# Kernel optimization log

Hardware: AMD Instinct MI355X
Metric: run time of the kernel (lower is better)

The kernel has to match this reference:

```python
import jax, jax.numpy as jnp
import numpy as np

B, S, D, H = 2, 2048, 1024, 16
HD = D // H  # head_dim = 64


def setup_inputs() -> dict:
    key = jax.random.key(0)
    ks = jax.random.split(key, 11)
    init = 1.0 / np.sqrt(D)
    inp = {
        "query": jax.random.normal(ks[0], (B, S, D), jnp.float32),
        "key": jax.random.normal(ks[1], (B, S, D), jnp.float32),
        "value": jax.random.normal(ks[2], (B, S, D), jnp.float32),
        "Wq": jax.random.uniform(ks[3], (D, D), jnp.float32, -init, init),
        "bq": jax.random.uniform(ks[4], (D,), jnp.float32, -init, init),
        "Wk": jax.random.uniform(ks[5], (D, D), jnp.float32, -init, init),
        "bk": jax.random.uniform(ks[6], (D,), jnp.float32, -init, init),
        "Wv": jax.random.uniform(ks[7], (D, D), jnp.float32, -init, init),
        "bv": jax.random.uniform(ks[8], (D,), jnp.float32, -init, init),
        "Wo": jax.random.uniform(ks[9], (D, D), jnp.float32, -init, init),
        "bo": jax.random.uniform(ks[10], (D,), jnp.float32, -init, init),
    }
    return inp


def reference(query, key, value, Wq, bq, Wk, bk, Wv, bv, Wo, bo):
    # Linear projections (torch Linear: x @ W.T + b)
    q = query @ Wq.T + bq  # [B,S,D]
    k = key @ Wk.T + bk
    v = value @ Wv.T + bv
    # split heads -> [B,H,S,HD]
    q = q.reshape(B, S, H, HD).transpose(0, 2, 1, 3)
    k = k.reshape(B, S, H, HD).transpose(0, 2, 1, 3)
    v = v.reshape(B, S, H, HD).transpose(0, 2, 1, 3)
    # NOTE: original code divides by scale = head_dim**-0.5, i.e. multiplies
    # scores by sqrt(head_dim). Reproduced faithfully.
    scale = HD ** (-0.5)
    scores = jnp.einsum("bhqd,bhkd->bhqk", q, k) / scale  # [B,H,S,S]
    attn = jax.nn.softmax(scores, axis=-1)
    x = jnp.einsum("bhqk,bhkd->bhqd", attn, v)  # [B,H,S,HD]
    x = x.transpose(0, 2, 1, 3).reshape(B, S, D)
    return x @ Wo.T + bo
```

## Files before the change

### kernel.cpp

```cpp
#include <hip/hip_runtime.h>
#include <stdint.h>
#include <stddef.h>

#define SCALE_LOG2E 11.541560327111707f
#define E8 4194304
#define M1 1048576
#define NROW 65536

typedef __attribute__((ext_vector_type(8))) _Float16 f16x8;
typedef __attribute__((ext_vector_type(4))) _Float16 f16x4;
typedef __attribute__((ext_vector_type(4))) float f32x4;

#if __has_builtin(__builtin_amdgcn_exp2f)
#define EXP2F(x) __builtin_amdgcn_exp2f(x)
#else
#define EXP2F(x) exp2f(x)
#endif

__device__ __forceinline__ f32x4 mfma_f16(f16x8 a, f16x8 b, f32x4 c) {
  return __builtin_amdgcn_mfma_f32_16x16x32_f16(a, b, c, 0, 0, 0);
}

__device__ __forceinline__ void async16(const void* g, void* lds) {
  __builtin_amdgcn_global_load_lds(
      (const __attribute__((address_space(1))) unsigned int*)g,
      (__attribute__((address_space(3))) unsigned int*)lds, 16, 0, 0);
}

__global__ void prep_all(const float* __restrict__ q, const float* __restrict__ k,
                         const float* __restrict__ v,
                         const float* __restrict__ wq, const float* __restrict__ wk,
                         const float* __restrict__ wv, const float* __restrict__ wo,
                         _Float16* __restrict__ Xf, _Float16* __restrict__ Wf) {
  const int gid = blockIdx.x;
  const float* src;
  _Float16* dst;
  int i;
  if (gid < 12288) {
    const int z = gid >> 12;
    src = (z == 0) ? q : (z == 1) ? k : v;
    dst = Xf + (size_t)z * E8;
    i = (gid & 4095) * 256 + threadIdx.x;
  } else {
    const int g2 = gid - 12288;
    const int z = g2 >> 10;
    src = (z == 0) ? wq : (z == 1) ? wk : (z == 2) ? wv : wo;
    dst = Wf + (size_t)z * M1;
    i = (g2 & 1023) * 256 + threadIdx.x;
  }
  float4 x = ((const float4*)src)[i];
  f16x4 h = {(_Float16)x.x, (_Float16)x.y, (_Float16)x.z, (_Float16)x.w};
  ((f16x4*)dst)[i] = h;
}

__global__ __launch_bounds__(256, 3) void gemm_qkv(
    const _Float16* __restrict__ Xf,
    const _Float16* __restrict__ Wf,
    const float* __restrict__ bq, const float* __restrict__ bk,
    const float* __restrict__ bv,
    _Float16* __restrict__ Of)
{
  __shared__ _Float16 SMEM[16384];
  _Float16* LA = SMEM;
  _Float16* LB = SMEM + 8192;
  const int z = blockIdx.z;
  const int tid = threadIdx.x;
  const int lane = tid & 63;
  const int wv = tid >> 6;
  const int wm = wv >> 1, wn = wv & 1;
  const int rl = lane & 15, qd = lane >> 4;
  const int m0 = blockIdx.y * 128, n0 = blockIdx.x * 128;

  const _Float16* A0 = Xf + (size_t)z * E8;
  const _Float16* W0 = Wf + (size_t)z * M1;
  const float* bias = (z == 0) ? bq : (z == 1) ? bk : bv;

  f32x4 acc[4][4];
#pragma unroll
  for (int i = 0; i < 4; i++)
#pragma unroll
    for (int j = 0; j < 4; j++) acc[i][j] = f32x4{0.f, 0.f, 0.f, 0.f};

  const int srow = wv * 32 + (lane >> 2);
  const int scol = (lane & 3) * 8;

  auto stage = [&](int k0, int buf) {
    const _Float16* ga = A0 + (size_t)(m0 + srow) * 1024 + k0 + scol;
    async16(ga, &LA[buf * 4096 + wv * 1024]);
    async16(ga + 16 * 1024, &LA[buf * 4096 + wv * 1024 + 512]);
    const _Float16* gb = W0 + (size_t)(n0 + srow) * 1024 + k0 + scol;
    async16(gb, &LB[buf * 4096 + wv * 1024]);
    async16(gb + 16 * 1024, &LB[buf * 4096 + wv * 1024 + 512]);
  };

  stage(0, 0);
  for (int t = 0; t < 32; t++) {
    const int buf = t & 1;
    __syncthreads();
    if (t + 1 < 32) stage((t + 1) * 32, buf ^ 1);
    f16x8 af[4], bfr[4];
#pragma unroll
    for (int i = 0; i < 4; i++) af[i] = *(const f16x8*)&LA[buf * 4096 + (wm * 64 + i * 16 + rl) * 32 + qd * 8];
#pragma unroll
    for (int j = 0; j < 4; j++) bfr[j] = *(const f16x8*)&LB[buf * 4096 + (wn * 64 + j * 16 + rl) * 32 + qd * 8];
#pragma unroll
    for (int i = 0; i < 4; i++)
#pragma unroll
      for (int j = 0; j < 4; j++) acc[i][j] = mfma_f16(af[i], bfr[j], acc[i][j]);
  }

  if (z == 2) {
#pragma unroll
    for (int j = 0; j < 4; j++) {
      const int nn = n0 + wn * 64 + j * 16 + rl;
      const float bj = bias[nn];
      const int hh = nn >> 6, e = nn & 63;
#pragma unroll
      for (int i = 0; i < 4; i++) {
        const int mm = m0 + wm * 64 + i * 16 + qd * 4;
        const int b = mm >> 11, s = mm & 2047;
        f16x4 pk = {(_Float16)(acc[i][j][0] + bj), (_Float16)(acc[i][j][1] + bj),
                    (_Float16)(acc[i][j][2] + bj), (_Float16)(acc[i][j][3] + bj)};
        *(f16x4*)(Of + 2 * (size_t)E8 + (((size_t)((b * 16 + hh) * 64 + e)) << 11) + s) = pk;
      }
    }
  } else {
    const float scl = (z == 0) ? SCALE_LOG2E : 1.0f;
    _Float16* base = Of + (size_t)z * E8;
    __syncthreads();
#pragma unroll
    for (int j = 0; j < 4; j++) {
      const int nl = wn * 64 + j * 16 + rl;
      const float bj = bias[n0 + nl];
#pragma unroll
      for (int i = 0; i < 4; i++) {
        const int ml = wm * 64 + i * 16 + qd * 4;
        const int np = nl ^ (qd << 4);
#pragma unroll
        for (int r = 0; r < 4; r++)
          SMEM[(ml + r) * 128 + np] = (_Float16)((acc[i][j][r] + bj) * scl);
      }
    }
    __syncthreads();
#pragma unroll
    for (int it2 = 0; it2 < 8; it2++) {
      const int m = (it2 * 256 + tid) >> 4;
      const int col8 = (tid & 15) * 8;
      const int np = col8 ^ (((m >> 2) & 3) << 4);
      f16x8 vrow = *(const f16x8*)&SMEM[m * 128 + np];
      const int sg = m0 + m;
      const int b = sg >> 11, s = sg & 2047;
      const int nn = n0 + col8;
      const int hh = nn >> 6, e = nn & 63;
      *(f16x8*)(base + (((size_t)((b * 16 + hh) * 2048 + s)) << 6) + e) = vrow;
    }
  }
}

__global__ __launch_bounds__(256, 3) void attn_kernel(
    const _Float16* __restrict__ Qb,
    const _Float16* __restrict__ Kb,
    const _Float16* __restrict__ Vt,
    float* __restrict__ Op,
    float2* __restrict__ ML)
{
  __shared__ _Float16 Ks[2][4096];
  __shared__ _Float16 Vs[2][4096];
  __shared__ _Float16 Ps[4][32][76];
  const int tid = threadIdx.x;
  const int lane = tid & 63;
  const int wv = tid >> 6;
  const int rl = lane & 15, qd = lane >> 4;
  const int bh = blockIdx.z;
  const int half = blockIdx.y;
  const int kvb = half * 1024;
  const int q0 = blockIdx.x * 128 + wv * 32;

  f16x8 qf[2][2];
#pragma unroll
  for (int mt = 0; mt < 2; mt++)
#pragma unroll
    for (int kk = 0; kk < 2; kk++)
      qf[mt][kk] = *(const f16x8*)(Qb + ((size_t)bh * 2048 + q0 + mt * 16 + rl) * 64 +
                                   kk * 32 + qd * 8);

  float m_[2] = {-1e30f, -1e30f}, l_[2] = {0.f, 0.f};
  f32x4 o[2][4];
#pragma unroll
  for (int mt = 0; mt < 2; mt++)
#pragma unroll
    for (int jt = 0; jt < 4; jt++) o[mt][jt] = f32x4{0.f, 0.f, 0.f, 0.f};

  auto stage = [&](int kv, int buf) {
#pragma unroll
    for (int it = 0; it < 2; it++) {
      const int cI = it * 256 + tid;
      const int row = cI >> 3;
      const int c = (cI & 7) ^ (row & 7);
      const int dst = (it * 256 + wv * 64) * 8;
      async16(Kb + ((size_t)bh * 2048 + kv + row) * 64 + c * 8, &Ks[buf][dst]);
      async16(Vt + ((size_t)bh * 64 + row) * 2048 + kv + c * 8, &Vs[buf][dst]);
    }
  };

  stage(kvb, 0);

  for (int t = 0; t < 16; t++) {
    const int buf = t & 1;
    __syncthreads();
    if (t + 1 < 16) stage(kvb + (t + 1) * 64, buf ^ 1);

    f32x4 sc[2][4];
#pragma unroll
    for (int mt = 0; mt < 2; mt++)
#pragma unroll
      for (int nt = 0; nt < 4; nt++) sc[mt][nt] = f32x4{0.f, 0.f, 0.f, 0.f};
#pragma unroll
    for (int nt = 0; nt < 4; nt++) {
      const int ro = (nt * 16 + rl) * 64;
#pragma unroll
      for (int kk = 0; kk < 2; kk++) {
        const int cc = (((kk * 4 + qd) ^ (rl & 7)) << 3);
        f16x8 kh = *(const f16x8*)&Ks[buf][ro + cc];
#pragma unroll
        for (int mt = 0; mt < 2; mt++)
          sc[mt][nt] = mfma_f16(kh, qf[mt][kk], sc[mt][nt]);
      }
    }

#pragma unroll
    for (int mt = 0; mt < 2; mt++) {
      float mloc = sc[mt][0][0];
#pragma unroll
      for (int nt = 0; nt < 4; nt++)
#pragma unroll
        for (int r = 0; r < 4; r++) mloc = fmaxf(mloc, sc[mt][nt][r]);
      float mx = fmaxf(mloc, __shfl_xor(mloc, 16));
      mx = fmaxf(mx, __shfl_xor(mx, 32));
      float sm = 0.f;
#pragma unroll
      for (int nt = 0; nt < 4; nt++)
#pragma unroll
        for (int r = 0; r < 4; r++) {
          float p = EXP2F(sc[mt][nt][r] - mloc);
          sc[mt][nt][r] = p;
          sm += p;
        }
      const float mold = m_[mt];
      const float mnew = fmaxf(mold, mx);
      m_[mt] = mnew;
      const float cf = EXP2F(mloc - mnew);
      if (__any(mnew > mold)) {
        const float al = EXP2F(mold - mnew);
        l_[mt] = l_[mt] * al + sm * cf;
#pragma unroll
        for (int jt = 0; jt < 4; jt++)
#pragma unroll
          for (int r = 0; r < 4; r++) o[mt][jt][r] *= al;
      } else {
        l_[mt] += sm * cf;
      }

#pragma unroll
      for (int nt = 0; nt < 4; nt++) {
        f16x4 pk = {(_Float16)(sc[mt][nt][0] * cf), (_Float16)(sc[mt][nt][1] * cf),
                    (_Float16)(sc[mt][nt][2] * cf), (_Float16)(sc[mt][nt][3] * cf)};
        *(f16x4*)&Ps[wv][mt * 16 + rl][nt * 16 + qd * 4] = pk;
      }
    }

#pragma unroll
    for (int kk2 = 0; kk2 < 2; kk2++) {
      f16x8 pf[2];
#pragma unroll
      for (int mt = 0; mt < 2; mt++)
        pf[mt] = *(const f16x8*)&Ps[wv][mt * 16 + rl][kk2 * 32 + qd * 8];
#pragma unroll
      for (int jt = 0; jt < 4; jt++) {
        const int cc = (((kk2 * 4 + qd) ^ (rl & 7)) << 3);
        f16x8 vv = *(const f16x8*)&Vs[buf][(jt * 16 + rl) * 64 + cc];
#pragma unroll
        for (int mt = 0; mt < 2; mt++)
          o[mt][jt] = mfma_f16(vv, pf[mt], o[mt][jt]);
      }
    }
  }

#pragma unroll
  for (int mt = 0; mt < 2; mt++) {
    float lt = l_[mt] + __shfl_xor(l_[mt], 16);
    lt += __shfl_xor(lt, 32);
    const size_t row = (size_t)bh * 2048 + q0 + mt * 16 + rl;
    float* op = Op + ((size_t)half * NROW + row) * 64;
#pragma unroll
    for (int jt = 0; jt < 4; jt++)
      *(f32x4*)(op + jt * 16 + qd * 4) = o[mt][jt];
    if (qd == 0) ML[(size_t)half * NROW + row] = make_float2(m_[mt], lt);
  }
}

__global__ void merge_kernel(const float* __restrict__ Op,
                             const float2* __restrict__ ML,
                             _Float16* __restrict__ Xo) {
  const int t = threadIdx.x;
  const int row = blockIdx.x * 16 + (t >> 4);
  const int d0 = (t & 15) * 4;
  const float2 ml1 = ML[row];
  const float2 ml2 = ML[NROW + row];
  const float m = fmaxf(ml1.x, ml2.x);
  const float w1 = EXP2F(ml1.x - m), w2 = EXP2F(ml2.x - m);
  const float inv = 1.0f / (ml1.y * w1 + ml2.y * w2);
  const float4 o1 = *(const float4*)(Op + (size_t)row * 64 + d0);
  const float4 o2 = *(const float4*)(Op + (size_t)NROW * 64 + (size_t)row * 64 + d0);
  const int bh = row >> 11, q = row & 2047;
  const int b = bh >> 4, hh = bh & 15;
  f16x4 pk = {(_Float16)((o1.x * w1 + o2.x * w2) * inv),
              (_Float16)((o1.y * w1 + o2.y * w2) * inv),
              (_Float16)((o1.z * w1 + o2.z * w2) * inv),
              (_Float16)((o1.w * w1 + o2.w * w2) * inv)};
  *(f16x4*)(Xo + ((size_t)(b * 2048 + q)) * 1024 + hh * 64 + d0) = pk;
}

__global__ __launch_bounds__(256, 2) void gemm_out(
    const _Float16* __restrict__ A0,
    const _Float16* __restrict__ W0,
    const float* __restrict__ bias,
    float* __restrict__ out)
{
  __shared__ _Float16 LA[2][2048];
  __shared__ _Float16 LB[2][4096];
  const int tid = threadIdx.x;
  const int lane = tid & 63;
  const int wv = tid >> 6;
  const int wm = wv >> 1, wn = wv & 1;
  const int rl = lane & 15, qd = lane >> 4;
  const int m0 = blockIdx.y * 64, n0 = blockIdx.x * 128;

  f32x4 acc[2][4];
#pragma unroll
  for (int i = 0; i < 2; i++)
#pragma unroll
    for (int j = 0; j < 4; j++) acc[i][j] = f32x4{0.f, 0.f, 0.f, 0.f};

  auto stage = [&](int k0, int buf) {
    {
      const int row = tid >> 2, c = tid & 3;
      async16(A0 + (size_t)(m0 + row) * 1024 + k0 + c * 8, &LA[buf][wv * 512]);
    }
#pragma unroll
    for (int it = 0; it < 2; it++) {
      const int cI = it * 256 + tid;
      const int row = cI >> 2, c = cI & 3;
      async16(W0 + (size_t)(n0 + row) * 1024 + k0 + c * 8,
              &LB[buf][it * 2048 + wv * 512]);
    }
  };

  stage(0, 0);
  for (int t = 0; t < 32; t++) {
    const int buf = t & 1;
    __syncthreads();
    if (t + 1 < 32) stage((t + 1) * 32, buf ^ 1);
    f16x8 af[2], bfr[4];
#pragma unroll
    for (int i = 0; i < 2; i++) af[i] = *(const f16x8*)&LA[buf][(wm * 32 + i * 16 + rl) * 32 + qd * 8];
#pragma unroll
    for (int j = 0; j < 4; j++) bfr[j] = *(const f16x8*)&LB[buf][(wn * 64 + j * 16 + rl) * 32 + qd * 8];
#pragma unroll
    for (int i = 0; i < 2; i++)
#pragma unroll
      for (int j = 0; j < 4; j++) acc[i][j] = mfma_f16(af[i], bfr[j], acc[i][j]);
  }

#pragma unroll
  for (int j = 0; j < 4; j++) {
    const int nn = n0 + wn * 64 + j * 16 + rl;
    const float bj = bias[nn];
#pragma unroll
    for (int i = 0; i < 2; i++) {
      const int mm = m0 + wm * 32 + i * 16 + qd * 4;
#pragma unroll
      for (int r = 0; r < 4; r++)
        out[(size_t)(mm + r) * 1024 + nn] = acc[i][j][r] + bj;
    }
  }
}

extern "C" void kernel_launch(void* const* d_in, const int* in_sizes, int n_in,
                              void* d_out, int out_size, void* d_ws, size_t ws_size,
                              hipStream_t stream) {
  const float* query = (const float*)d_in[0];
  const float* key   = (const float*)d_in[1];
  const float* value = (const float*)d_in[2];
  const float* Wq = (const float*)d_in[3];
  const float* bq = (const float*)d_in[4];
  const float* Wk = (const float*)d_in[5];
  const float* bk = (const float*)d_in[6];
  const float* Wv = (const float*)d_in[7];
  const float* bv = (const float*)d_in[8];
  const float* Wo = (const float*)d_in[9];
  const float* bo = (const float*)d_in[10];

  _Float16* ws = (_Float16*)d_ws;
  _Float16* Xf = ws;
  _Float16* Wf = ws + 3 * (size_t)E8;
  _Float16* Qh = Wf + 4 * (size_t)M1;
  _Float16* Kh = Qh + (size_t)E8;
  _Float16* Vt = Kh + (size_t)E8;
  _Float16* Xa = Vt + (size_t)E8;
  float*    Op = (float*)(Xa + (size_t)E8);
  float2*   ML = (float2*)(Op + 2 * (size_t)NROW * 64);

  prep_all<<<16384, 256, 0, stream>>>(query, key, value, Wq, Wk, Wv, Wo, Xf, Wf);
  gemm_qkv<<<dim3(8, 32, 3), 256, 0, stream>>>(Xf, Wf, bq, bk, bv, Qh);
  attn_kernel<<<dim3(16, 2, 32), 256, 0, stream>>>(Qh, Kh, Vt, Op, ML);
  merge_kernel<<<4096, 256, 0, stream>>>(Op, ML, Xa);
  gemm_out<<<dim3(8, 64), 256, 0, stream>>>(Xa, Wf + 3 * (size_t)M1, bo, (float*)d_out);
}
```

Measured before the change: 245.4 us.

## Keep P in registers via 16x16x16 MFMA, lazy rescale, raise occupancy

Removes the per-wave LDS staging of the softmax probabilities: the score accumulator layout is fed directly as the B operand of 16x16x16 f16 MFMAs for the PV product, with V read in matching 4-element chunks. Adds a lazy max-rescale that only updates the running max when it grows by more than 8 (log2 units). Also raises launch bounds to 4 waves-per-EU occupancy and wraps MFMA sections in s_setprio. This trades LDS traffic and barriers-free shuffles for twice as many smaller MFMAs, and the lazy threshold risks fp16 overflow of exp values up to 2^8 per element.

```diff
diff --git a/kernel.cpp b/kernel.cpp
--- a/kernel.cpp
+++ b/kernel.cpp
@@ -19,6 +19,10 @@
 
 __device__ __forceinline__ f32x4 mfma_f16(f16x8 a, f16x8 b, f32x4 c) {
   return __builtin_amdgcn_mfma_f32_16x16x32_f16(a, b, c, 0, 0, 0);
+}
+
+__device__ __forceinline__ f32x4 mfma16_f16(f16x4 a, f16x4 b, f32x4 c) {
+  return __builtin_amdgcn_mfma_f32_16x16x16f16(a, b, c, 0, 0, 0);
 }
 
 __device__ __forceinline__ void async16(const void* g, void* lds) {
@@ -157,7 +161,7 @@
   }
 }
 
-__global__ __launch_bounds__(256, 3) void attn_kernel(
+__global__ __launch_bounds__(256, 4) void attn_kernel(
     const _Float16* __restrict__ Qb,
     const _Float16* __restrict__ Kb,
     const _Float16* __restrict__ Vt,
@@ -166,7 +170,6 @@
 {
   __shared__ _Float16 Ks[2][4096];
   __shared__ _Float16 Vs[2][4096];
-  __shared__ _Float16 Ps[4][32][76];
   const int tid = threadIdx.x;
   const int lane = tid & 63;
   const int wv = tid >> 6;
@@ -215,6 +218,7 @@
     for (int mt = 0; mt < 2; mt++)
 #pragma unroll
       for (int nt = 0; nt < 4; nt++) sc[mt][nt] = f32x4{0.f, 0.f, 0.f, 0.f};
+    __builtin_amdgcn_s_setprio(1);
 #pragma unroll
     for (int nt = 0; nt < 4; nt++) {
       const int ro = (nt * 16 + rl) * 64;
@@ -227,63 +231,56 @@
           sc[mt][nt] = mfma_f16(kh, qf[mt][kk], sc[mt][nt]);
       }
     }
-
+    __builtin_amdgcn_s_setprio(0);
+
+    f16x4 pf[2][4];
 #pragma unroll
     for (int mt = 0; mt < 2; mt++) {
-      float mloc = sc[mt][0][0];
-#pragma unroll
-      for (int nt = 0; nt < 4; nt++)
-#pragma unroll
-        for (int r = 0; r < 4; r++) mloc = fmaxf(mloc, sc[mt][nt][r]);
+      float a0 = fmaxf(fmaxf(sc[mt][0][0], sc[mt][0][1]), fmaxf(sc[mt][0][2], sc[mt][0][3]));
+      float a1 = fmaxf(fmaxf(sc[mt][1][0], sc[mt][1][1]), fmaxf(sc[mt][1][2], sc[mt][1][3]));
+      float a2 = fmaxf(fmaxf(sc[mt][2][0], sc[mt][2][1]), fmaxf(sc[mt][2][2], sc[mt][2][3]));
+      float a3 = fmaxf(fmaxf(sc[mt][3][0], sc[mt][3][1]), fmaxf(sc[mt][3][2], sc[mt][3][3]));
+      float mloc = fmaxf(fmaxf(a0, a1), fmaxf(a2, a3));
       float mx = fmaxf(mloc, __shfl_xor(mloc, 16));
       mx = fmaxf(mx, __shfl_xor(mx, 32));
+      const float mold = m_[mt];
+      float mnew = mold;
+      if (__any(mx > mold + 8.f)) {
+        mnew = fmaxf(mold, mx);
+        const float al = EXP2F(mold - mnew);
+        l_[mt] *= al;
+#pragma unroll
+        for (int jt = 0; jt < 4; jt++)
+#pragma unroll
+          for (int r = 0; r < 4; r++) o[mt][jt][r] *= al;
+        m_[mt] = mnew;
+      }
       float sm = 0.f;
 #pragma unroll
-      for (int nt = 0; nt < 4; nt++)
-#pragma unroll
-        for (int r = 0; r < 4; r++) {
-          float p = EXP2F(sc[mt][nt][r] - mloc);
-          sc[mt][nt][r] = p;
-          sm += p;
-        }
-      const float mold = m_[mt];
-      const float mnew = fmaxf(mold, mx);
-      m_[mt] = mnew;
-      const float cf = EXP2F(mloc - mnew);
-      if (__any(mnew > mold)) {
-        const float al = EXP2F(mold - mnew);
-        l_[mt] = l_[mt] * al + sm * cf;
-#pragma unroll
-        for (int jt = 0; jt < 4; jt++)
-#pragma unroll
-          for (int r = 0; r < 4; r++) o[mt][jt][r] *= al;
-      } else {
-        l_[mt] += sm * cf;
-      }
-
-#pragma unroll
       for (int nt = 0; nt < 4; nt++) {
-        f16x4 pk = {(_Float16)(sc[mt][nt][0] * cf), (_Float16)(sc[mt][nt][1] * cf),
-                    (_Float16)(sc[mt][nt][2] * cf), (_Float16)(sc[mt][nt][3] * cf)};
-        *(f16x4*)&Ps[wv][mt * 16 + rl][nt * 16 + qd * 4] = pk;
-      }
-    }
-
-#pragma unroll
-    for (int kk2 = 0; kk2 < 2; kk2++) {
-      f16x8 pf[2];
-#pragma unroll
-      for (int mt = 0; mt < 2; mt++)
-        pf[mt] = *(const f16x8*)&Ps[wv][mt * 16 + rl][kk2 * 32 + qd * 8];
+        const float p0 = EXP2F(sc[mt][nt][0] - mnew);
+        const float p1 = EXP2F(sc[mt][nt][1] - mnew);
+        const float p2 = EXP2F(sc[mt][nt][2] - mnew);
+        const float p3 = EXP2F(sc[mt][nt][3] - mnew);
+        sm += (p0 + p1) + (p2 + p3);
+        pf[mt][nt] = f16x4{(_Float16)p0, (_Float16)p1, (_Float16)p2, (_Float16)p3};
+      }
+      l_[mt] += sm;
+    }
+
+    __builtin_amdgcn_s_setprio(1);
+#pragma unroll
+    for (int nt = 0; nt < 4; nt++) {
+      const int cb = nt * 2 + (qd >> 1);
 #pragma unroll
       for (int jt = 0; jt < 4; jt++) {
-        const int cc = (((kk2 * 4 + qd) ^ (rl & 7)) << 3);
-        f16x8 vv = *(const f16x8*)&Vs[buf][(jt * 16 + rl) * 64 + cc];
-#pragma unroll
-        for (int mt = 0; mt < 2; mt++)
-          o[mt][jt] = mfma_f16(vv, pf[mt], o[mt][jt]);
-      }
-    }
+        const int row = jt * 16 + rl;
+        f16x4 vvv = *(const f16x4*)&Vs[buf][row * 64 + ((cb ^ (rl & 7)) << 3) + (qd & 1) * 4];
+        o[0][jt] = mfma16_f16(vvv, pf[0][nt], o[0][jt]);
+        o[1][jt] = mfma16_f16(vvv, pf[1][nt], o[1][jt]);
+      }
+    }
+    __builtin_amdgcn_s_setprio(0);
   }
 
 #pragma unroll
```

New measurement: 249.8 us. Within noise of the previous version (+1.8%).
